# Kernel tuning notes

Hardware: AMD Instinct MI355X
Metric: run time of the kernel (lower is better)

The kernel has to match this reference:

```python
import jax, jax.numpy as jnp
import numpy as np

EMBED_DIM = 1024
NUM_HEADS = 16
D_K = EMBED_DIM // NUM_HEADS


def setup_inputs() -> dict:
    key = jax.random.key(0)
    ks = jax.random.split(key, 9)
    s = 1.0 / np.sqrt(EMBED_DIM)
    x = jax.random.normal(ks[0], (4, 2048, EMBED_DIM), dtype=jnp.float32)
    # nn.Linear weights stored as [out, in]; we keep [in, out] for x @ W
    W_q = jax.random.uniform(ks[1], (EMBED_DIM, EMBED_DIM), jnp.float32, -s, s)
    b_q = jax.random.uniform(ks[2], (EMBED_DIM,), jnp.float32, -s, s)
    W_k = jax.random.uniform(ks[3], (EMBED_DIM, EMBED_DIM), jnp.float32, -s, s)
    b_k = jax.random.uniform(ks[4], (EMBED_DIM,), jnp.float32, -s, s)
    W_v = jax.random.uniform(ks[5], (EMBED_DIM, EMBED_DIM), jnp.float32, -s, s)
    b_v = jax.random.uniform(ks[6], (EMBED_DIM,), jnp.float32, -s, s)
    W_o = jax.random.uniform(ks[7], (EMBED_DIM, EMBED_DIM), jnp.float32, -s, s)
    b_o = jax.random.uniform(ks[8], (EMBED_DIM,), jnp.float32, -s, s)
    return {"x": x, "W_q": W_q, "b_q": b_q, "W_k": W_k, "b_k": b_k,
            "W_v": W_v, "b_v": b_v, "W_o": W_o, "b_o": b_o}


def reference(x, W_q, b_q, W_k, b_k, W_v, b_v, W_o, b_o):
    B, N, _ = x.shape
    # QKV projections, split into heads: [B, H, N, d_k]
    def proj(W, b):
        return (x @ W + b).reshape(B, N, NUM_HEADS, D_K).transpose(0, 2, 1, 3)
    Q, K, V = proj(W_q, b_q), proj(W_k, b_k), proj(W_v, b_v)
    scale = 1.0 / np.sqrt(D_K).astype(np.float32)
    scores = jnp.einsum('bhqd,bhkd->bhqk', Q, K) * scale  # [B,H,N,N]
    weights = jax.nn.softmax(scores, axis=-1)
    # dropout is identity in eval mode
    attn = jnp.einsum('bhqk,bhkd->bhqd', weights, V)  # [B,H,N,d_k]
    attn = attn.transpose(0, 2, 1, 3).reshape(B, N, EMBED_DIM)
    return attn @ W_o + b_o
```

## Files before the change

### kernel.cpp

```cpp
#include <hip/hip_runtime.h>

typedef __bf16 bf16;
typedef __attribute__((ext_vector_type(8))) __bf16 bf16x8;
typedef __attribute__((ext_vector_type(4))) __bf16 bf16x4;
typedef __attribute__((ext_vector_type(4))) float f32x4;

static __device__ __forceinline__ f32x4 mfma16(bf16x8 a, bf16x8 b, f32x4 c) {
    return __builtin_amdgcn_mfma_f32_16x16x32_bf16(a, b, c, 0, 0, 0);
}

static __device__ __forceinline__ void gll16(const bf16* g, bf16* l) {
    __builtin_amdgcn_global_load_lds(
        (const __attribute__((address_space(1))) unsigned int*)g,
        (__attribute__((address_space(3))) unsigned int*)l, 16, 0, 0);
}

__global__ __launch_bounds__(256) void xcvt_kernel(
    const float* __restrict__ x, bf16* __restrict__ xb)
{
    size_t i = ((size_t)blockIdx.x * 256 + threadIdx.x) * 8;
    float4 a0 = *(const float4*)&x[i];
    float4 a1 = *(const float4*)&x[i + 4];
    bf16x8 v = {(bf16)a0.x, (bf16)a0.y, (bf16)a0.z, (bf16)a0.w,
                (bf16)a1.x, (bf16)a1.y, (bf16)a1.z, (bf16)a1.w};
    *(bf16x8*)&xb[i] = v;
}

__global__ __launch_bounds__(256) void wtrans_kernel(
    const float* __restrict__ Wq, const float* __restrict__ Wk,
    const float* __restrict__ Wv, const float* __restrict__ Wo,
    bf16* __restrict__ WTqkv, bf16* __restrict__ WTo)
{
    __shared__ bf16 tile[64][65];
    const int bid = blockIdx.x;
    const int mi = bid >> 8;
    const int t  = bid & 255;
    const int tr = t >> 4;
    const int tc = t & 15;
    const int tid = threadIdx.x;

    const float* src = (mi == 0) ? Wq : (mi == 1) ? Wk : (mi == 2) ? Wv : Wo;
    bf16* dst = (mi < 3) ? (WTqkv + (size_t)mi * 1024 * 1024) : WTo;

    #pragma unroll
    for (int i = 0; i < 16; i++) {
        int idx = i * 256 + tid;
        int rl = idx >> 6, cl = idx & 63;
        tile[rl][cl] = (bf16)src[(size_t)(tr * 64 + rl) * 1024 + tc * 64 + cl];
    }
    __syncthreads();
    #pragma unroll
    for (int i = 0; i < 16; i++) {
        int idx = i * 256 + tid;
        int rl = idx >> 6, cl = idx & 63;
        dst[(size_t)(tc * 64 + rl) * 1024 + tr * 64 + cl] = tile[cl][rl];
    }
}

__global__ void biascat_kernel(const float* __restrict__ bq, const float* __restrict__ bk,
                               const float* __restrict__ bv, float* __restrict__ dst)
{
    int i = blockIdx.x * 256 + threadIdx.x;
    if (i < 1024) dst[i] = bq[i];
    else if (i < 2048) dst[i] = bk[i - 1024];
    else dst[i] = bv[i - 2048];
}

#define QSCALE 0.18033688011112043f
__global__ __launch_bounds__(256) void gemm_bf16_kernel(
    const bf16* __restrict__ A, const bf16* __restrict__ BT,
    const float* __restrict__ bias, bf16* __restrict__ C,
    int M, int N, int K, int scaleQ)
{
    __shared__ bf16 sA[128 * 32];
    __shared__ bf16 sB[128 * 32];
    const int tid  = threadIdx.x;
    const int lane = tid & 63;
    const int wave = tid >> 6;
    const int quad = lane >> 4;
    const int l15  = lane & 15;
    const int wm = (wave >> 1) * 64;
    const int wn = (wave & 1) * 64;
    const int m0 = blockIdx.y * 128;
    const int n0 = blockIdx.x * 128;

    const f32x4 fzero = {0.f, 0.f, 0.f, 0.f};
    f32x4 acc[4][4];
    #pragma unroll
    for (int i = 0; i < 4; i++)
        #pragma unroll
        for (int j = 0; j < 4; j++) acc[i][j] = fzero;

    float bv[4];
    #pragma unroll
    for (int nc = 0; nc < 4; nc++) bv[nc] = bias[n0 + wn + nc * 16 + l15];

    const int rA = lane >> 2;
    const int cA = (lane & 3) * 8;

    for (int k0 = 0; k0 < K; k0 += 32) {
        #pragma unroll
        for (int p = 0; p < 2; p++) {
            int r16 = (wave * 2 + p) * 16;
            gll16(&A[(size_t)(m0 + r16 + rA) * K + k0 + cA], &sA[r16 * 32]);
            gll16(&BT[(size_t)(n0 + r16 + rA) * K + k0 + cA], &sB[r16 * 32]);
        }
        __syncthreads();

        bf16x8 aF[4], bF[4];
        #pragma unroll
        for (int mc = 0; mc < 4; mc++)
            aF[mc] = *(const bf16x8*)&sA[(wm + mc * 16 + l15) * 32 + quad * 8];
        #pragma unroll
        for (int nc = 0; nc < 4; nc++)
            bF[nc] = *(const bf16x8*)&sB[(wn + nc * 16 + l15) * 32 + quad * 8];

        #pragma unroll
        for (int mc = 0; mc < 4; mc++)
            #pragma unroll
            for (int nc = 0; nc < 4; nc++)
                acc[mc][nc] = mfma16(aF[mc], bF[nc], acc[mc][nc]);
        __syncthreads();
    }

    const float sc = (scaleQ && n0 < 1024) ? QSCALE : 1.0f;
    #pragma unroll
    for (int mc = 0; mc < 4; mc++) {
        #pragma unroll
        for (int reg = 0; reg < 4; reg++) {
            int row = m0 + wm + mc * 16 + quad * 4 + reg;
            size_t base = (size_t)row * N + n0 + wn;
            #pragma unroll
            for (int nc = 0; nc < 4; nc++)
                C[base + nc * 16 + l15] = (bf16)((acc[mc][nc][reg] + bv[nc]) * sc);
        }
    }
}

__global__ __launch_bounds__(256) void gemm_bf16_f32out_kernel(
    const bf16* __restrict__ A, const bf16* __restrict__ BT,
    const float* __restrict__ bias, float* __restrict__ C,
    int M, int N, int K)
{
    __shared__ bf16 sA[128 * 32];
    __shared__ bf16 sB[128 * 32];
    const int tid  = threadIdx.x;
    const int lane = tid & 63;
    const int wave = tid >> 6;
    const int quad = lane >> 4;
    const int l15  = lane & 15;
    const int wm = (wave >> 1) * 64;
    const int wn = (wave & 1) * 64;
    const int m0 = blockIdx.y * 128;
    const int n0 = blockIdx.x * 128;

    const f32x4 fzero = {0.f, 0.f, 0.f, 0.f};
    f32x4 acc[4][4];
    #pragma unroll
    for (int i = 0; i < 4; i++)
        #pragma unroll
        for (int j = 0; j < 4; j++) acc[i][j] = fzero;

    float bv[4];
    #pragma unroll
    for (int nc = 0; nc < 4; nc++) bv[nc] = bias[n0 + wn + nc * 16 + l15];

    const int rA = lane >> 2;
    const int cA = (lane & 3) * 8;

    for (int k0 = 0; k0 < K; k0 += 32) {
        #pragma unroll
        for (int p = 0; p < 2; p++) {
            int r16 = (wave * 2 + p) * 16;
            gll16(&A[(size_t)(m0 + r16 + rA) * K + k0 + cA], &sA[r16 * 32]);
            gll16(&BT[(size_t)(n0 + r16 + rA) * K + k0 + cA], &sB[r16 * 32]);
        }
        __syncthreads();

        bf16x8 aF[4], bF[4];
        #pragma unroll
        for (int mc = 0; mc < 4; mc++)
            aF[mc] = *(const bf16x8*)&sA[(wm + mc * 16 + l15) * 32 + quad * 8];
        #pragma unroll
        for (int nc = 0; nc < 4; nc++)
            bF[nc] = *(const bf16x8*)&sB[(wn + nc * 16 + l15) * 32 + quad * 8];

        #pragma unroll
        for (int mc = 0; mc < 4; mc++)
            #pragma unroll
            for (int nc = 0; nc < 4; nc++)
                acc[mc][nc] = mfma16(aF[mc], bF[nc], acc[mc][nc]);
        __syncthreads();
    }

    #pragma unroll
    for (int mc = 0; mc < 4; mc++) {
        #pragma unroll
        for (int reg = 0; reg < 4; reg++) {
            int row = m0 + wm + mc * 16 + quad * 4 + reg;
            size_t base = (size_t)row * N + n0 + wn;
            #pragma unroll
            for (int nc = 0; nc < 4; nc++)
                C[base + nc * 16 + l15] = acc[mc][nc][reg] + bv[nc];
        }
    }
}

__global__ __launch_bounds__(256) void vtrans_kernel(
    const bf16* __restrict__ QKVp, bf16* __restrict__ Vt)
{
    __shared__ bf16 tile[64][65];
    const int bid = blockIdx.x;
    const int bh = bid >> 5;
    const int nt = bid & 31;
    const int b = bh >> 4, h = bh & 15;
    const int tid = threadIdx.x;

    #pragma unroll
    for (int i = 0; i < 16; i++) {
        int idx = i * 256 + tid;
        int rl = idx >> 6, cl = idx & 63;
        tile[rl][cl] = QKVp[(size_t)(b * 2048 + nt * 64 + rl) * 3072 + 2048 + h * 64 + cl];
    }
    __syncthreads();
    #pragma unroll
    for (int i = 0; i < 16; i++) {
        int idx = i * 256 + tid;
        int rl = idx >> 6, cl = idx & 63;
        Vt[((size_t)bh * 64 + rl) * 2048 + nt * 64 + cl] = tile[cl][rl];
    }
}

__global__ __launch_bounds__(256) void attn_kernel(
    const bf16* __restrict__ QKV, const bf16* __restrict__ Vt,
    bf16* __restrict__ Opre)
{
    __shared__ bf16 sK[2][64 * 64];
    __shared__ bf16 sV[2][64 * 64];

    const int tid  = threadIdx.x;
    const int lane = tid & 63;
    const int w    = tid >> 6;
    const int quad = lane >> 4;
    const int l15  = lane & 15;
    const int bid = (blockIdx.x & 7) * 128 + (blockIdx.x >> 3);
    const int bh = bid >> 4;
    const int qt = bid & 15;
    const int b = bh >> 4, h = bh & 15;
    const int q0 = qt * 128;

    bf16x8 qF[2][2];
    #pragma unroll
    for (int g = 0; g < 2; g++) {
        size_t qrow = (size_t)(b * 2048 + q0 + w * 32 + g * 16 + l15) * 3072 + h * 64;
        qF[g][0] = *(const bf16x8*)&QKV[qrow + quad * 8];
        qF[g][1] = *(const bf16x8*)&QKV[qrow + 32 + quad * 8];
    }

    const f32x4 fzero = {0.f, 0.f, 0.f, 0.f};
    const bf16 one = (bf16)1.0f;
    const bf16x8 ones = {one, one, one, one, one, one, one, one};
    f32x4 ps[2] = {fzero, fzero};
    f32x4 o[2][4];
    #pragma unroll
    for (int g = 0; g < 2; g++)
        #pragma unroll
        for (int mt = 0; mt < 4; mt++) o[g][mt] = fzero;

    const int srow = tid >> 3, sseg = tid & 7;
    const size_t kbase = (size_t)(b * 2048) * 3072 + 1024 + h * 64;
    const size_t vbase = (size_t)bh * 64 * 2048;
    const int sgsw = sseg ^ ((srow & 3) | (((srow >> 3) & 1) << 2));

    const int swk = (l15 & 3) | (((l15 >> 2) & 1) << 2);
    const int swv = (l15 & 3) | (((l15 >> 3) & 1) << 2);

    bf16x8 stAK[2], stAV[2], stBK[2], stBV[2];

#define ISSUE(RK, RV, KEY0)                                                       \
    _Pragma("unroll")                                                             \
    for (int p = 0; p < 2; p++) {                                                 \
        int row = srow + p * 32;                                                  \
        RK[p] = *(const bf16x8*)&QKV[kbase + (size_t)((KEY0) + row) * 3072 + sseg * 8]; \
        RV[p] = *(const bf16x8*)&Vt[vbase + (size_t)row * 2048 + (KEY0) + sseg * 8];    \
    }

#define COMMIT(RK, RV, BUF)                                                       \
    _Pragma("unroll")                                                             \
    for (int p = 0; p < 2; p++) {                                                 \
        int row = srow + p * 32;                                                  \
        *(bf16x8*)&sK[BUF][row * 64 + sgsw * 8] = RK[p];                          \
        *(bf16x8*)&sV[BUF][row * 64 + sgsw * 8] = RV[p];                          \
    }

    auto compute_tile = [&](const bf16* sKc, const bf16* sVc) {
        bf16x8 pB[2][2];
        #pragma unroll
        for (int c = 0; c < 4; c++) {
            int kr = ((l15 >> 2) << 3) + ((c & 1) << 2) + (l15 & 3) + ((c >> 1) << 5);
            bf16x8 kA0 = *(const bf16x8*)&sKc[kr * 64 + ((quad ^ swk) * 8)];
            bf16x8 kA1 = *(const bf16x8*)&sKc[kr * 64 + (((4 + quad) ^ swk) * 8)];
            #pragma unroll
            for (int g = 0; g < 2; g++) {
                __builtin_amdgcn_s_setprio(1);
                f32x4 st = mfma16(kA0, qF[g][0], fzero);
                st = mfma16(kA1, qF[g][1], st);
                __builtin_amdgcn_s_setprio(0);
                #pragma unroll
                for (int r = 0; r < 4; r++) {
                    float p = __builtin_amdgcn_exp2f(st[r]);
                    pB[g][c >> 1][(c & 1) * 4 + r] = (bf16)p;
                }
            }
        }
        __builtin_amdgcn_s_setprio(1);
        #pragma unroll
        for (int g = 0; g < 2; g++) {
            ps[g] = mfma16(ones, pB[g][0], ps[g]);
            ps[g] = mfma16(ones, pB[g][1], ps[g]);
        }
        __builtin_amdgcn_s_setprio(0);
        #pragma unroll
        for (int mt = 0; mt < 4; mt++) {
            int vr = mt * 16 + l15;
            bf16x8 vA0 = *(const bf16x8*)&sVc[vr * 64 + ((quad ^ swv) * 8)];
            bf16x8 vA1 = *(const bf16x8*)&sVc[vr * 64 + (((4 + quad) ^ swv) * 8)];
            __builtin_amdgcn_s_setprio(1);
            #pragma unroll
            for (int g = 0; g < 2; g++) {
                o[g][mt] = mfma16(vA0, pB[g][0], o[g][mt]);
                o[g][mt] = mfma16(vA1, pB[g][1], o[g][mt]);
            }
            __builtin_amdgcn_s_setprio(0);
        }
    };

    ISSUE(stAK, stAV, 0);
    ISSUE(stBK, stBV, 64);
    COMMIT(stAK, stAV, 0);
    __syncthreads();

    for (int t = 0; t < 30; t += 2) {
        ISSUE(stAK, stAV, (t + 2) * 64);
        __builtin_amdgcn_sched_barrier(0);
        compute_tile(sK[0], sV[0]);
        COMMIT(stBK, stBV, 1);
        __syncthreads();

        ISSUE(stBK, stBV, (t + 3) * 64);
        __builtin_amdgcn_sched_barrier(0);
        compute_tile(sK[1], sV[1]);
        COMMIT(stAK, stAV, 0);
        __syncthreads();
    }
    compute_tile(sK[0], sV[0]);
    COMMIT(stBK, stBV, 1);
    __syncthreads();
    compute_tile(sK[1], sV[1]);

#undef ISSUE
#undef COMMIT

    #pragma unroll
    for (int g = 0; g < 2; g++) {
        float inv = 1.0f / ps[g][0];
        size_t obase = (size_t)(b * 2048 + q0 + w * 32 + g * 16 + l15) * 1024 + h * 64;
        #pragma unroll
        for (int mt = 0; mt < 4; mt++) {
            bf16x4 ov = {(bf16)(o[g][mt][0] * inv), (bf16)(o[g][mt][1] * inv),
                         (bf16)(o[g][mt][2] * inv), (bf16)(o[g][mt][3] * inv)};
            *(bf16x4*)&Opre[obase + mt * 16 + quad * 4] = ov;
        }
    }
}

extern "C" void kernel_launch(void* const* d_in, const int* in_sizes, int n_in,
                              void* d_out, int out_size, void* d_ws, size_t ws_size,
                              hipStream_t stream)
{
    const float* x  = (const float*)d_in[0];
    const float* Wq = (const float*)d_in[1];
    const float* bq = (const float*)d_in[2];
    const float* Wk = (const float*)d_in[3];
    const float* bk = (const float*)d_in[4];
    const float* Wv = (const float*)d_in[5];
    const float* bv = (const float*)d_in[6];
    const float* Wo = (const float*)d_in[7];
    const float* bo = (const float*)d_in[8];
    float* out = (float*)d_out;

    bf16* WTqkv = (bf16*)d_ws;
    bf16* WTo   = WTqkv + (size_t)3072 * 1024;
    float* bcat = (float*)(WTo + (size_t)1024 * 1024);
    bf16* QKVp  = (bf16*)(bcat + 4096);
    bf16* Vt    = QKVp + (size_t)8192 * 3072;
    bf16* Apre  = Vt + (size_t)64 * 64 * 2048;
    bf16* xb    = Apre;
    (void)ws_size; (void)n_in; (void)in_sizes; (void)out_size;

    xcvt_kernel<<<4096, 256, 0, stream>>>(x, xb);
    wtrans_kernel<<<1024, 256, 0, stream>>>(Wq, Wk, Wv, Wo, WTqkv, WTo);
    biascat_kernel<<<12, 256, 0, stream>>>(bq, bk, bv, bcat);
    gemm_bf16_kernel<<<dim3(24, 64), 256, 0, stream>>>(xb, WTqkv, bcat, QKVp, 8192, 3072, 1024, 1);
    vtrans_kernel<<<2048, 256, 0, stream>>>(QKVp, Vt);
    attn_kernel<<<1024, 256, 0, stream>>>(QKVp, Vt, Apre);
    gemm_bf16_f32out_kernel<<<dim3(8, 64), 256, 0, stream>>>(Apre, WTo, bo, out, 8192, 1024, 1024);
}
```

Baseline: 299.8 us.

## Halve attention block to two waves, each handling 64 query rows

The attention kernel now launches 128 threads per block instead of 256. Each wave processes four 16-row query groups instead of two, so every K/V fragment read from LDS feeds twice as many MFMAs. The staging pipeline moves from two register sets (A/B) to a single set with a one-tile lookahead. The cost is much higher register use per wave (double accumulators and P fragments) and fewer waves per block, which may reduce latency hiding. Per-thread global load count also doubles.

```diff
diff --git a/kernel.cpp b/kernel.cpp
--- a/kernel.cpp
+++ b/kernel.cpp
@@ -231,7 +231,7 @@
     }
 }
 
-__global__ __launch_bounds__(256) void attn_kernel(
+__global__ __launch_bounds__(128, 2) void attn_kernel(
     const bf16* __restrict__ QKV, const bf16* __restrict__ Vt,
     bf16* __restrict__ Opre)
 {
@@ -249,10 +249,10 @@
     const int b = bh >> 4, h = bh & 15;
     const int q0 = qt * 128;
 
-    bf16x8 qF[2][2];
-    #pragma unroll
-    for (int g = 0; g < 2; g++) {
-        size_t qrow = (size_t)(b * 2048 + q0 + w * 32 + g * 16 + l15) * 3072 + h * 64;
+    bf16x8 qF[4][2];
+    #pragma unroll
+    for (int g = 0; g < 4; g++) {
+        size_t qrow = (size_t)(b * 2048 + q0 + w * 64 + g * 16 + l15) * 3072 + h * 64;
         qF[g][0] = *(const bf16x8*)&QKV[qrow + quad * 8];
         qF[g][1] = *(const bf16x8*)&QKV[qrow + 32 + quad * 8];
     }
@@ -260,10 +260,10 @@
     const f32x4 fzero = {0.f, 0.f, 0.f, 0.f};
     const bf16 one = (bf16)1.0f;
     const bf16x8 ones = {one, one, one, one, one, one, one, one};
-    f32x4 ps[2] = {fzero, fzero};
-    f32x4 o[2][4];
-    #pragma unroll
-    for (int g = 0; g < 2; g++)
+    f32x4 ps[4] = {fzero, fzero, fzero, fzero};
+    f32x4 o[4][4];
+    #pragma unroll
+    for (int g = 0; g < 4; g++)
         #pragma unroll
         for (int mt = 0; mt < 4; mt++) o[g][mt] = fzero;
 
@@ -275,33 +275,33 @@
     const int swk = (l15 & 3) | (((l15 >> 2) & 1) << 2);
     const int swv = (l15 & 3) | (((l15 >> 3) & 1) << 2);
 
-    bf16x8 stAK[2], stAV[2], stBK[2], stBV[2];
-
-#define ISSUE(RK, RV, KEY0)                                                       \
+    bf16x8 stK[4], stV[4];
+
+#define ISSUE(KEY0)                                                               \
     _Pragma("unroll")                                                             \
-    for (int p = 0; p < 2; p++) {                                                 \
-        int row = srow + p * 32;                                                  \
-        RK[p] = *(const bf16x8*)&QKV[kbase + (size_t)((KEY0) + row) * 3072 + sseg * 8]; \
-        RV[p] = *(const bf16x8*)&Vt[vbase + (size_t)row * 2048 + (KEY0) + sseg * 8];    \
-    }
-
-#define COMMIT(RK, RV, BUF)                                                       \
+    for (int p = 0; p < 4; p++) {                                                 \
+        int row = srow + p * 16;                                                  \
+        stK[p] = *(const bf16x8*)&QKV[kbase + (size_t)((KEY0) + row) * 3072 + sseg * 8]; \
+        stV[p] = *(const bf16x8*)&Vt[vbase + (size_t)row * 2048 + (KEY0) + sseg * 8];    \
+    }
+
+#define COMMIT(BUF)                                                               \
     _Pragma("unroll")                                                             \
-    for (int p = 0; p < 2; p++) {                                                 \
-        int row = srow + p * 32;                                                  \
-        *(bf16x8*)&sK[BUF][row * 64 + sgsw * 8] = RK[p];                          \
-        *(bf16x8*)&sV[BUF][row * 64 + sgsw * 8] = RV[p];                          \
+    for (int p = 0; p < 4; p++) {                                                 \
+        int row = srow + p * 16;                                                  \
+        *(bf16x8*)&sK[BUF][row * 64 + sgsw * 8] = stK[p];                         \
+        *(bf16x8*)&sV[BUF][row * 64 + sgsw * 8] = stV[p];                         \
     }
 
     auto compute_tile = [&](const bf16* sKc, const bf16* sVc) {
-        bf16x8 pB[2][2];
+        bf16x8 pB[4][2];
         #pragma unroll
         for (int c = 0; c < 4; c++) {
             int kr = ((l15 >> 2) << 3) + ((c & 1) << 2) + (l15 & 3) + ((c >> 1) << 5);
             bf16x8 kA0 = *(const bf16x8*)&sKc[kr * 64 + ((quad ^ swk) * 8)];
             bf16x8 kA1 = *(const bf16x8*)&sKc[kr * 64 + (((4 + quad) ^ swk) * 8)];
             #pragma unroll
-            for (int g = 0; g < 2; g++) {
+            for (int g = 0; g < 4; g++) {
                 __builtin_amdgcn_s_setprio(1);
                 f32x4 st = mfma16(kA0, qF[g][0], fzero);
                 st = mfma16(kA1, qF[g][1], st);
@@ -315,7 +315,7 @@
         }
         __builtin_amdgcn_s_setprio(1);
         #pragma unroll
-        for (int g = 0; g < 2; g++) {
+        for (int g = 0; g < 4; g++) {
             ps[g] = mfma16(ones, pB[g][0], ps[g]);
             ps[g] = mfma16(ones, pB[g][1], ps[g]);
         }
@@ -327,7 +327,7 @@
             bf16x8 vA1 = *(const bf16x8*)&sVc[vr * 64 + (((4 + quad) ^ swv) * 8)];
             __builtin_amdgcn_s_setprio(1);
             #pragma unroll
-            for (int g = 0; g < 2; g++) {
+            for (int g = 0; g < 4; g++) {
                 o[g][mt] = mfma16(vA0, pB[g][0], o[g][mt]);
                 o[g][mt] = mfma16(vA1, pB[g][1], o[g][mt]);
             }
@@ -335,36 +335,26 @@
         }
     };
 
-    ISSUE(stAK, stAV, 0);
-    ISSUE(stBK, stBV, 64);
-    COMMIT(stAK, stAV, 0);
+    ISSUE(0);
+    COMMIT(0);
     __syncthreads();
 
-    for (int t = 0; t < 30; t += 2) {
-        ISSUE(stAK, stAV, (t + 2) * 64);
+    for (int t = 0; t < 31; t++) {
+        ISSUE((t + 1) * 64);
         __builtin_amdgcn_sched_barrier(0);
-        compute_tile(sK[0], sV[0]);
-        COMMIT(stBK, stBV, 1);
-        __syncthreads();
-
-        ISSUE(stBK, stBV, (t + 3) * 64);
-        __builtin_amdgcn_sched_barrier(0);
-        compute_tile(sK[1], sV[1]);
-        COMMIT(stAK, stAV, 0);
-        __syncthreads();
-    }
-    compute_tile(sK[0], sV[0]);
-    COMMIT(stBK, stBV, 1);
-    __syncthreads();
+        compute_tile(sK[t & 1], sV[t & 1]);
+        COMMIT((t + 1) & 1);
+        __syncthreads();
+    }
     compute_tile(sK[1], sV[1]);
 
 #undef ISSUE
 #undef COMMIT
 
     #pragma unroll
-    for (int g = 0; g < 2; g++) {
+    for (int g = 0; g < 4; g++) {
         float inv = 1.0f / ps[g][0];
-        size_t obase = (size_t)(b * 2048 + q0 + w * 32 + g * 16 + l15) * 1024 + h * 64;
+        size_t obase = (size_t)(b * 2048 + q0 + w * 64 + g * 16 + l15) * 1024 + h * 64;
         #pragma unroll
         for (int mt = 0; mt < 4; mt++) {
             bf16x4 ov = {(bf16)(o[g][mt][0] * inv), (bf16)(o[g][mt][1] * inv),
@@ -403,6 +393,6 @@
     biascat_kernel<<<12, 256, 0, stream>>>(bq, bk, bv, bcat);
     gemm_bf16_kernel<<<dim3(24, 64), 256, 0, stream>>>(xb, WTqkv, bcat, QKVp, 8192, 3072, 1024, 1);
     vtrans_kernel<<<2048, 256, 0, stream>>>(QKVp, Vt);
-    attn_kernel<<<1024, 256, 0, stream>>>(QKVp, Vt, Apre);
+    attn_kernel<<<1024, 128, 0, stream>>>(QKVp, Vt, Apre);
     gemm_bf16_f32out_kernel<<<dim3(8, 64), 256, 0, stream>>>(Apre, WTo, bo, out, 8192, 1024, 1024);
 }
```

Result: faster. 286.7 us (-4.4%).
